# Kernel optimization log

Hardware: AMD Instinct MI355X
Metric: run time of the kernel (lower is better)

Reference implementation:

```python
import jax, jax.numpy as jnp
import numpy as np

NEG_SLOPE = 0.2


def gat_conv(h_in, src, dst, W, attn_l, attn_r, num_nodes):
    """DGL-style GATConv: fc -> per-head attention logits -> edge softmax over dst -> scatter-add."""
    H, D = attn_l.shape
    h = (h_in @ W).reshape(num_nodes, H, D)                      # [N,H,D]
    el = jnp.sum(h * attn_l, axis=-1)                            # [N,H]
    er = jnp.sum(h * attn_r, axis=-1)                            # [N,H]
    e = jax.nn.leaky_relu(el[src] + er[dst], NEG_SLOPE)          # [E,H]
    m = jax.ops.segment_max(e, dst, num_segments=num_nodes)      # [N,H]
    m = jnp.where(jnp.isfinite(m), m, 0.0)                       # guard empty segments
    ex = jnp.exp(e - m[dst])                                     # [E,H]
    denom = jax.ops.segment_sum(ex, dst, num_segments=num_nodes) # [N,H]
    a = ex / denom[dst]                                          # [E,H]
    msg = h[src] * a[:, :, None]                                 # [E,H,D]
    out = jax.ops.segment_sum(msg, dst, num_segments=num_nodes)  # [N,H,D]
    return out.reshape(num_nodes, H * D)                         # concat heads


def setup_inputs() -> dict:
    key = jax.random.key(0)
    ks = jax.random.split(key, 12)
    N, E, G = 65536, 1048576, 512
    F_in, H, D = 128, 8, 32
    F_mid = H * D  # 256, concat agg mode
    P = 512
    inp = {
        "node_feats": jax.random.normal(ks[0], (N, F_in), jnp.float32),
        "src": jax.random.randint(ks[1], (E,), 0, N, jnp.int32),
        "dst": jax.random.randint(ks[2], (E,), 0, N, jnp.int32),
        "graph_ids": jnp.sort(jax.random.randint(ks[3], (N,), 0, G, jnp.int32)),
        "num_graphs": G,
        "W0": jax.random.normal(ks[4], (F_in, H * D), jnp.float32) * (1.0 / np.sqrt(F_in)),
        "al0": jax.random.normal(ks[5], (H, D), jnp.float32) * 0.1,
        "ar0": jax.random.normal(ks[6], (H, D), jnp.float32) * 0.1,
        "W1": jax.random.normal(ks[7], (F_mid, H * D), jnp.float32) * (1.0 / np.sqrt(F_mid)),
        "al1": jax.random.normal(ks[8], (H, D), jnp.float32) * 0.1,
        "ar1": jax.random.normal(ks[9], (H, D), jnp.float32) * 0.1,
        "Wd1": jax.random.normal(ks[10], (F_mid, P), jnp.float32) * (1.0 / np.sqrt(F_mid)),
        "bd1": jnp.zeros((P,), jnp.float32),
        "Wd2": jax.random.normal(ks[11], (P, 1), jnp.float32) * (1.0 / np.sqrt(P)),
        "bd2": jnp.zeros((1,), jnp.float32),
    }
    return inp


def reference(node_feats, src, dst, graph_ids, num_graphs,
              W0, al0, ar0, W1, al1, ar1, Wd1, bd1, Wd2, bd2):
    N = node_feats.shape[0]
    # two GATConv message-passing steps with concat head aggregation
    h = gat_conv(node_feats, src, dst, W0, al0, ar0, N)   # [N, 256]
    h = gat_conv(h, src, dst, W1, al1, ar1, N)            # [N, 256]
    # mean readout per graph (AvgPooling)
    sums = jax.ops.segment_sum(h, graph_ids, num_segments=num_graphs)         # [G, 256]
    counts = jax.ops.segment_sum(jnp.ones((N,), h.dtype), graph_ids,
                                 num_segments=num_graphs)                     # [G]
    pooled = sums / jnp.maximum(counts, 1.0)[:, None]
    # predictor MLP: Dense(512, relu) -> Dense(1, linear)
    hidden = jax.nn.relu(pooled @ Wd1 + bd1)
    out = hidden @ Wd2 + bd2                               # [G, 1]
    return out
```

## Files before the change

kernel.cpp:

```cpp
#include <hip/hip_runtime.h>

#define LEAKY 0.2f

typedef unsigned short ushort_t;
typedef __attribute__((ext_vector_type(8))) short short8;
typedef __attribute__((ext_vector_type(4))) float f32x4;

__device__ __forceinline__ unsigned short f2bf(float f) {
  unsigned u = __float_as_uint(f);
  unsigned r = (u + 0x7fff + ((u >> 16) & 1)) >> 16;
  return (unsigned short)r;
}
__device__ __forceinline__ float bf2f(unsigned short u) {
  return __uint_as_float(((unsigned)u) << 16);
}

__global__ __launch_bounds__(256) void prep_k(int* __restrict__ cnt,
                                              const float* __restrict__ W0,
                                              const float* __restrict__ W1,
                                              ushort_t* __restrict__ W0h,
                                              ushort_t* __restrict__ W1h, int N) {
  int i = blockIdx.x * 256 + threadIdx.x;
  if (i < N) cnt[i] = 0;
  if (i < 256 * 128) {
    int k = i % 128, c = i / 128;
    W0h[i] = f2bf(W0[(long)k * 256 + c]);
  }
  if (i < 256 * 256) {
    int k = i % 256, c = i / 256;
    W1h[i] = f2bf(W1[(long)k * 256 + c]);
  }
}

__global__ void count_k(const int* __restrict__ dst, int* __restrict__ cnt,
                        int* __restrict__ slot, int E) {
  int base = (blockIdx.x * blockDim.x + threadIdx.x) * 4;
  if (base + 3 < E) {
    int4 d = *(const int4*)(dst + base);
    int4 s;
    s.x = atomicAdd(&cnt[d.x], 1);
    s.y = atomicAdd(&cnt[d.y], 1);
    s.z = atomicAdd(&cnt[d.z], 1);
    s.w = atomicAdd(&cnt[d.w], 1);
    *(int4*)(slot + base) = s;
  } else {
    for (int i = base; i < E; ++i) slot[i] = atomicAdd(&cnt[dst[i]], 1);
  }
}

__global__ __launch_bounds__(1024) void scan1_k(const int* __restrict__ cnt,
                                                int* __restrict__ ptr,
                                                int* __restrict__ bsum, int N) {
  int t = threadIdx.x;
  int i = blockIdx.x * 1024 + t;
  int v = (i < N) ? cnt[i] : 0;
  int lane = t & 63, w = t >> 6;
  int x = v;
  #pragma unroll
  for (int off = 1; off < 64; off <<= 1) {
    int y = __shfl_up(x, off, 64);
    if (lane >= off) x += y;
  }
  __shared__ int wsum[16];
  if (lane == 63) wsum[w] = x;
  __syncthreads();
  if (t < 16) {
    int s = wsum[t];
    #pragma unroll
    for (int off = 1; off < 16; off <<= 1) {
      int y = __shfl_up(s, off, 16);
      if (t >= off) s += y;
    }
    wsum[t] = s;
  }
  __syncthreads();
  int woff = (w > 0) ? wsum[w - 1] : 0;
  int incl = x + woff;
  if (i < N) ptr[i] = incl - v;
  if (t == 1023) bsum[blockIdx.x] = incl;
}

__global__ __launch_bounds__(1024) void scan23_k(int* __restrict__ ptr,
                                                 const int* __restrict__ bsum,
                                                 int nb, int N, int E) {
  __shared__ int sh[64];
  int t = threadIdx.x;
  if (t < 64) {
    int v = (t < nb) ? bsum[t] : 0;
    int x = v;
    #pragma unroll
    for (int off = 1; off < 64; off <<= 1) {
      int y = __shfl_up(x, off, 64);
      if (t >= off) x += y;
    }
    sh[t] = x - v;
  }
  __syncthreads();
  int i = blockIdx.x * 1024 + t;
  if (i < N) ptr[i] += sh[blockIdx.x];
  if (i == 0) ptr[N] = E;
}

__global__ void fill_k(const int* __restrict__ dst, const int* __restrict__ src,
                       const int* __restrict__ slot, const int* __restrict__ ptr,
                       int* __restrict__ adj, int E) {
  int base = (blockIdx.x * blockDim.x + threadIdx.x) * 4;
  if (base + 3 < E) {
    int4 d = *(const int4*)(dst + base);
    int4 s = *(const int4*)(src + base);
    int4 q = *(const int4*)(slot + base);
    adj[ptr[d.x] + q.x] = s.x;
    adj[ptr[d.y] + q.y] = s.y;
    adj[ptr[d.z] + q.z] = s.z;
    adj[ptr[d.w] + q.w] = s.w;
  } else {
    for (int i = base; i < E; ++i) adj[ptr[dst[i]] + slot[i]] = src[i];
  }
}

#define LDT 40
template <int AF32>
__global__ __launch_bounds__(256) void gemmT_k(const void* __restrict__ Ag_,
                                               const ushort_t* __restrict__ Bh,
                                               const float* __restrict__ alv,
                                               const float* __restrict__ arv,
                                               ushort_t* __restrict__ C,
                                               float* __restrict__ el,
                                               float* __restrict__ er,
                                               int N, int K) {
  __shared__ ushort_t smem[128 * LDT + 256 * LDT];
  ushort_t* As = smem;
  ushort_t* Bs = smem + 128 * LDT;
  int t = threadIdx.x;
  int w = t >> 6, l = t & 63;
  int wv_r = w >> 1, wv_c = w & 1;
  long row0 = (long)blockIdx.x * 128;
  int fr = l & 15;
  int ko = (l >> 4) * 8;
  int crow = (l >> 4) * 4;
  int ar = t >> 1;
  int ak = (t & 1) * 16;
  int bc = t;
  f32x4 acc[4][8] = {};

  for (int k0 = 0; k0 < K; k0 += 32) {
    ushort4 ha[4];
    uint4 a0, a1;
    if (AF32) {
      const float* ap = (const float*)Ag_ + (row0 + ar) * (long)K + k0 + ak;
      float4 v0 = *(const float4*)(ap + 0);
      float4 v1 = *(const float4*)(ap + 4);
      float4 v2 = *(const float4*)(ap + 8);
      float4 v3 = *(const float4*)(ap + 12);
      ha[0] = make_ushort4(f2bf(v0.x), f2bf(v0.y), f2bf(v0.z), f2bf(v0.w));
      ha[1] = make_ushort4(f2bf(v1.x), f2bf(v1.y), f2bf(v1.z), f2bf(v1.w));
      ha[2] = make_ushort4(f2bf(v2.x), f2bf(v2.y), f2bf(v2.z), f2bf(v2.w));
      ha[3] = make_ushort4(f2bf(v3.x), f2bf(v3.y), f2bf(v3.z), f2bf(v3.w));
    } else {
      const ushort_t* ap = (const ushort_t*)Ag_ + (row0 + ar) * (long)K + k0 + ak;
      a0 = *(const uint4*)ap;
      a1 = *(const uint4*)(ap + 8);
    }
    const ushort_t* bp = Bh + (long)bc * K + k0;
    uint4 b0 = *(const uint4*)bp;
    uint4 b1 = *(const uint4*)(bp + 8);
    uint4 b2 = *(const uint4*)(bp + 16);
    uint4 b3 = *(const uint4*)(bp + 24);
    __syncthreads();
    if (AF32) {
      *(ushort4*)&As[ar * LDT + ak + 0] = ha[0];
      *(ushort4*)&As[ar * LDT + ak + 4] = ha[1];
      *(ushort4*)&As[ar * LDT + ak + 8] = ha[2];
      *(ushort4*)&As[ar * LDT + ak + 12] = ha[3];
    } else {
      *(uint4*)&As[ar * LDT + ak] = a0;
      *(uint4*)&As[ar * LDT + ak + 8] = a1;
    }
    *(uint4*)&Bs[bc * LDT + 0] = b0;
    *(uint4*)&Bs[bc * LDT + 8] = b1;
    *(uint4*)&Bs[bc * LDT + 16] = b2;
    *(uint4*)&Bs[bc * LDT + 24] = b3;
    __syncthreads();
    short8 fah[4];
    #pragma unroll
    for (int m = 0; m < 4; ++m)
      fah[m] = *(const short8*)&As[(wv_r * 64 + m * 16 + fr) * LDT + ko];
    #pragma unroll
    for (int n = 0; n < 8; ++n) {
      short8 fb = *(const short8*)&Bs[(wv_c * 128 + n * 16 + fr) * LDT + ko];
      #pragma unroll
      for (int m = 0; m < 4; ++m)
        acc[m][n] = __builtin_amdgcn_mfma_f32_16x16x32_bf16(fah[m], fb, acc[m][n], 0, 0, 0);
    }
  }
  float ala[4], alb[4], ara[4], arb[4];
  #pragma unroll
  for (int hd = 0; hd < 4; ++hd) {
    int hbase = (wv_c * 4 + hd) * 32;
    ala[hd] = alv[hbase + fr];
    alb[hd] = alv[hbase + 16 + fr];
    ara[hd] = arv[hbase + fr];
    arb[hd] = arv[hbase + 16 + fr];
  }
  #pragma unroll
  for (int m = 0; m < 4; ++m) {
    #pragma unroll
    for (int r = 0; r < 4; ++r) {
      long row = row0 + wv_r * 64 + m * 16 + crow + r;
      #pragma unroll
      for (int n = 0; n < 8; ++n)
        C[row * 256 + wv_c * 128 + n * 16 + fr] = f2bf(acc[m][n][r]);
      #pragma unroll
      for (int hd = 0; hd < 4; ++hd) {
        float pel = acc[m][2 * hd][r] * ala[hd] + acc[m][2 * hd + 1][r] * alb[hd];
        float per = acc[m][2 * hd][r] * ara[hd] + acc[m][2 * hd + 1][r] * arb[hd];
        #pragma unroll
        for (int s = 1; s < 16; s <<= 1) {
          pel += __shfl_xor(pel, s);
          per += __shfl_xor(per, s);
        }
        if (fr == 0) {
          el[row * 8 + wv_c * 4 + hd] = pel;
          er[row * 8 + wv_c * 4 + hd] = per;
        }
      }
    }
  }
}

__global__ __launch_bounds__(256) void agg_k(const ushort_t* __restrict__ hb,
                                             const float* __restrict__ el,
                                             const float* __restrict__ er,
                                             const int* __restrict__ ptr,
                                             const int* __restrict__ adj,
                                             ushort_t* __restrict__ oh, int N) {
  __shared__ float2 att[4][64][8];
  int wid = threadIdx.x >> 6;
  int l = threadIdx.x & 63;
  int n = blockIdx.x * 4 + wid;
  if (n >= N) return;
  int beg = ptr[n];
  int deg = ptr[n + 1] - beg;
  long obase = (long)n * 256 + l * 4;
  float4 acc = make_float4(0.f, 0.f, 0.f, 0.f);
  if (deg > 0) {
    int hh = l & 7;
    int eo = l >> 3;
    int hg = l >> 3;
    float erv = er[(long)n * 8 + hh];
    if (deg <= 64) {
      int sid = (l < deg) ? adj[beg + l] : 0;
      int npass = (deg + 7) >> 3;
      float v[8];
      int sv[8];
      float m = -1e30f;
      #pragma unroll
      for (int p = 0; p < 8; ++p) {
        if (p < npass) {
          int e = p * 8 + eo;
          int s = __shfl(sid, e);
          sv[p] = s;
          float vv = -1e30f;
          if (e < deg) {
            vv = el[(long)s * 8 + hh] + erv;
            vv = fmaxf(vv, LEAKY * vv);
          }
          v[p] = vv;
          m = fmaxf(m, vv);
        }
      }
      m = fmaxf(m, __shfl_xor(m, 8));
      m = fmaxf(m, __shfl_xor(m, 16));
      m = fmaxf(m, __shfl_xor(m, 32));
      float ssum = 0.f;
      #pragma unroll
      for (int p = 0; p < 8; ++p) {
        if (p < npass) {
          float ex = (p * 8 + eo < deg) ? __expf(v[p] - m) : 0.f;
          v[p] = ex;
          ssum += ex;
        }
      }
      ssum += __shfl_xor(ssum, 8);
      ssum += __shfl_xor(ssum, 16);
      ssum += __shfl_xor(ssum, 32);
      float inv = 1.0f / ssum;
      #pragma unroll
      for (int p = 0; p < 8; ++p) {
        if (p < npass) {
          int e = p * 8 + eo;
          if (e < deg)
            att[wid][e][hh] = make_float2(v[p] * inv, __int_as_float(sv[p]));
        }
      }
      for (int p = 0; p < npass; ++p) {
        #pragma unroll
        for (int e2 = 0; e2 < 8; ++e2) {
          int e = p * 8 + e2;
          if (e < deg) {
            float2 as_ = att[wid][e][hg];
            float a = as_.x;
            int s = __float_as_int(as_.y);
            const ushort4 hv = *(const ushort4*)(hb + (long)s * 256 + l * 4);
            acc.x += a * bf2f(hv.x);
            acc.y += a * bf2f(hv.y);
            acc.z += a * bf2f(hv.z);
            acc.w += a * bf2f(hv.w);
          }
        }
      }
    } else {
      float m = -1e30f;
      for (int base = 0; base < deg; base += 8) {
        int e = base + eo;
        float vv = -1e30f;
        if (e < deg) {
          int s = adj[beg + e];
          vv = el[(long)s * 8 + hh] + erv;
          vv = fmaxf(vv, LEAKY * vv);
        }
        m = fmaxf(m, vv);
      }
      m = fmaxf(m, __shfl_xor(m, 8));
      m = fmaxf(m, __shfl_xor(m, 16));
      m = fmaxf(m, __shfl_xor(m, 32));
      float ssum = 0.f;
      for (int base = 0; base < deg; base += 8) {
        int e = base + eo;
        if (e < deg) {
          int s = adj[beg + e];
          float vv = el[(long)s * 8 + hh] + erv;
          vv = fmaxf(vv, LEAKY * vv);
          ssum += __expf(vv - m);
        }
      }
      ssum += __shfl_xor(ssum, 8);
      ssum += __shfl_xor(ssum, 16);
      ssum += __shfl_xor(ssum, 32);
      float inv = 1.0f / ssum;
      for (int base = 0; base < deg; base += 8) {
        int e = base + eo;
        float a_me = 0.f;
        int s_me = 0;
        if (e < deg) {
          s_me = adj[beg + e];
          float vv = el[(long)s_me * 8 + hh] + erv;
          vv = fmaxf(vv, LEAKY * vv);
          a_me = __expf(vv - m) * inv;
        }
        #pragma unroll
        for (int e2 = 0; e2 < 8; ++e2) {
          int e3 = base + e2;
          if (e3 < deg) {
            int srcl = (e2 << 3) | hg;
            float a = __shfl(a_me, srcl);
            int s = __shfl(s_me, srcl);
            const ushort4 hv = *(const ushort4*)(hb + (long)s * 256 + l * 4);
            acc.x += a * bf2f(hv.x);
            acc.y += a * bf2f(hv.y);
            acc.z += a * bf2f(hv.z);
            acc.w += a * bf2f(hv.w);
          }
        }
      }
    }
  }
  *(ushort4*)(oh + obase) =
      make_ushort4(f2bf(acc.x), f2bf(acc.y), f2bf(acc.z), f2bf(acc.w));
}

__device__ __forceinline__ int lower_bound_i(const int* a, int n, int key) {
  int lo = 0, hi = n;
  while (lo < hi) {
    int mid = (lo + hi) >> 1;
    if (a[mid] < key) lo = mid + 1; else hi = mid;
  }
  return lo;
}

__global__ __launch_bounds__(256) void poolmlp_k(const ushort_t* __restrict__ h,
                                                 const int* __restrict__ gid,
                                                 const float* __restrict__ Wd1,
                                                 const float* __restrict__ bd1,
                                                 const float* __restrict__ Wd2,
                                                 const float* __restrict__ bd2,
                                                 float* __restrict__ outv, int N, int G) {
  int g = blockIdx.x;
  int t = threadIdx.x;
  __shared__ int s_lo, s_hi;
  if (t == 0) {
    s_lo = lower_bound_i(gid, N, g);
    s_hi = lower_bound_i(gid, N, g + 1);
  }
  __syncthreads();
  int lo = s_lo, hi = s_hi;
  float acc = 0.f;
  for (int n = lo; n < hi; ++n) acc += bf2f(h[(long)n * 256 + t]);
  float c = (float)(hi - lo);
  __shared__ float p_s[256];
  __shared__ float red[256];
  p_s[t] = acc / fmaxf(c, 1.f);
  __syncthreads();
  float acc0 = bd1[t], acc1 = bd1[t + 256];
  for (int k = 0; k < 256; ++k) {
    float pv = p_s[k];
    acc0 += pv * Wd1[k * 512 + t];
    acc1 += pv * Wd1[k * 512 + t + 256];
  }
  acc0 = fmaxf(acc0, 0.f);
  acc1 = fmaxf(acc1, 0.f);
  red[t] = acc0 * Wd2[t] + acc1 * Wd2[t + 256];
  __syncthreads();
  for (int off = 128; off > 0; off >>= 1) {
    if (t < off) red[t] += red[t + off];
    __syncthreads();
  }
  if (t == 0) outv[g] = red[0] + bd2[0];
}

extern "C" void kernel_launch(void* const* d_in, const int* in_sizes, int n_in,
                              void* d_out, int out_size, void* d_ws, size_t ws_size,
                              hipStream_t stream) {
  const float* X   = (const float*)d_in[0];
  const int*   src = (const int*)d_in[1];
  const int*   dst = (const int*)d_in[2];
  const int*   gid = (const int*)d_in[3];
  const float* W0  = (const float*)d_in[5];
  const float* al0 = (const float*)d_in[6];
  const float* ar0 = (const float*)d_in[7];
  const float* W1  = (const float*)d_in[8];
  const float* al1 = (const float*)d_in[9];
  const float* ar1 = (const float*)d_in[10];
  const float* Wd1 = (const float*)d_in[11];
  const float* bd1 = (const float*)d_in[12];
  const float* Wd2 = (const float*)d_in[13];
  const float* bd2 = (const float*)d_in[14];

  int E = in_sizes[1];
  int N = in_sizes[3];
  int G = out_size;

  char* p = (char*)d_ws;
  ushort_t* hb   = (ushort_t*)p; p += (size_t)N * 256 * 2;
  ushort_t* hagg = (ushort_t*)p; p += (size_t)N * 256 * 2;
  float*    el   = (float*)p;    p += (size_t)N * 8 * 4;
  float*    er   = (float*)p;    p += (size_t)N * 8 * 4;
  ushort_t* W0h  = (ushort_t*)p; p += (size_t)256 * 128 * 2;
  ushort_t* W1h  = (ushort_t*)p; p += (size_t)256 * 256 * 2;
  int*      ptr  = (int*)p;      p += (size_t)(N + 1) * 4;
  int*      cnt  = (int*)p;      p += (size_t)N * 4;
  int*      adj  = (int*)p;      p += (size_t)E * 4;
  int*      slot = (int*)p;      p += (size_t)E * 4;
  int*      bsum = (int*)p;

  int nb = (N + 1023) / 1024;

  prep_k<<<(N + 255) / 256, 256, 0, stream>>>(cnt, W0, W1, W0h, W1h, N);
  count_k<<<(E / 4 + 255) / 256, 256, 0, stream>>>(dst, cnt, slot, E);
  scan1_k<<<nb, 1024, 0, stream>>>(cnt, ptr, bsum, N);
  scan23_k<<<nb, 1024, 0, stream>>>(ptr, bsum, nb, N, E);
  fill_k<<<(E / 4 + 255) / 256, 256, 0, stream>>>(dst, src, slot, ptr, adj, E);

  gemmT_k<1><<<N / 128, 256, 0, stream>>>((const void*)X, W0h, al0, ar0, hb, el, er, N, 128);
  agg_k<<<(N + 3) / 4, 256, 0, stream>>>(hb, el, er, ptr, adj, hagg, N);
  gemmT_k<0><<<N / 128, 256, 0, stream>>>((const void*)hagg, W1h, al1, ar1, hb, el, er, N, 256);
  agg_k<<<(N + 3) / 4, 256, 0, stream>>>(hb, el, er, ptr, adj, hagg, N);
  poolmlp_k<<<G, 256, 0, stream>>>(hagg, gid, Wd1, bd1, Wd2, bd2, (float*)d_out, N, G);
}
```

Before: 415.5 us.

## Merge adjacency fill into first GEMM launch and use shuffles in aggregation

The CSR fill kernel becomes extra blocks inside the first GEMM launch, which removes one launch and lets the fill overlap with the GEMM. In the aggregation kernel, the low-degree path now broadcasts attention weights and source ids through wave shuffles instead of staging them in LDS, which frees shared memory and drops a store/load round trip. The pooling loop is unrolled by four with independent accumulators to expose more memory-level parallelism. The leaky ReLU is rewritten as a select. Fill blocks still reserve the GEMM's shared-memory allocation, which may limit how many can be resident at once.

```diff
diff --git a/kernel.cpp b/kernel.cpp
--- a/kernel.cpp
+++ b/kernel.cpp
@@ -101,25 +101,8 @@
   if (i == 0) ptr[N] = E;
 }
 
-__global__ void fill_k(const int* __restrict__ dst, const int* __restrict__ src,
-                       const int* __restrict__ slot, const int* __restrict__ ptr,
-                       int* __restrict__ adj, int E) {
-  int base = (blockIdx.x * blockDim.x + threadIdx.x) * 4;
-  if (base + 3 < E) {
-    int4 d = *(const int4*)(dst + base);
-    int4 s = *(const int4*)(src + base);
-    int4 q = *(const int4*)(slot + base);
-    adj[ptr[d.x] + q.x] = s.x;
-    adj[ptr[d.y] + q.y] = s.y;
-    adj[ptr[d.z] + q.z] = s.z;
-    adj[ptr[d.w] + q.w] = s.w;
-  } else {
-    for (int i = base; i < E; ++i) adj[ptr[dst[i]] + slot[i]] = src[i];
-  }
-}
-
 #define LDT 40
-template <int AF32>
+template <int AF32, int FILL>
 __global__ __launch_bounds__(256) void gemmT_k(const void* __restrict__ Ag_,
                                                const ushort_t* __restrict__ Bh,
                                                const float* __restrict__ alv,
@@ -127,8 +110,28 @@
                                                ushort_t* __restrict__ C,
                                                float* __restrict__ el,
                                                float* __restrict__ er,
-                                               int N, int K) {
+                                               int N, int K, int gemmBlocks,
+                                               const int* __restrict__ dstv,
+                                               const int* __restrict__ srcv,
+                                               const int* __restrict__ slot,
+                                               const int* __restrict__ ptrc,
+                                               int* __restrict__ adj, int E) {
   __shared__ ushort_t smem[128 * LDT + 256 * LDT];
+  if (FILL && blockIdx.x >= gemmBlocks) {
+    int base = ((blockIdx.x - gemmBlocks) * 256 + threadIdx.x) * 4;
+    if (base + 3 < E) {
+      int4 d = *(const int4*)(dstv + base);
+      int4 s = *(const int4*)(srcv + base);
+      int4 q = *(const int4*)(slot + base);
+      adj[ptrc[d.x] + q.x] = s.x;
+      adj[ptrc[d.y] + q.y] = s.y;
+      adj[ptrc[d.z] + q.z] = s.z;
+      adj[ptrc[d.w] + q.w] = s.w;
+    } else {
+      for (int i = base; i < E; ++i) adj[ptrc[dstv[i]] + slot[i]] = srcv[i];
+    }
+    return;
+  }
   ushort_t* As = smem;
   ushort_t* Bs = smem + 128 * LDT;
   int t = threadIdx.x;
@@ -234,7 +237,6 @@
                                              const int* __restrict__ ptr,
                                              const int* __restrict__ adj,
                                              ushort_t* __restrict__ oh, int N) {
-  __shared__ float2 att[4][64][8];
   int wid = threadIdx.x >> 6;
   int l = threadIdx.x & 63;
   int n = blockIdx.x * 4 + wid;
@@ -252,18 +254,16 @@
       int sid = (l < deg) ? adj[beg + l] : 0;
       int npass = (deg + 7) >> 3;
       float v[8];
-      int sv[8];
       float m = -1e30f;
       #pragma unroll
       for (int p = 0; p < 8; ++p) {
         if (p < npass) {
           int e = p * 8 + eo;
           int s = __shfl(sid, e);
-          sv[p] = s;
           float vv = -1e30f;
           if (e < deg) {
             vv = el[(long)s * 8 + hh] + erv;
-            vv = fmaxf(vv, LEAKY * vv);
+            vv = vv > 0.f ? vv : LEAKY * vv;
           }
           v[p] = vv;
           m = fmaxf(m, vv);
@@ -288,24 +288,19 @@
       #pragma unroll
       for (int p = 0; p < 8; ++p) {
         if (p < npass) {
-          int e = p * 8 + eo;
-          if (e < deg)
-            att[wid][e][hh] = make_float2(v[p] * inv, __int_as_float(sv[p]));
-        }
-      }
-      for (int p = 0; p < npass; ++p) {
-        #pragma unroll
-        for (int e2 = 0; e2 < 8; ++e2) {
-          int e = p * 8 + e2;
-          if (e < deg) {
-            float2 as_ = att[wid][e][hg];
-            float a = as_.x;
-            int s = __float_as_int(as_.y);
-            const ushort4 hv = *(const ushort4*)(hb + (long)s * 256 + l * 4);
-            acc.x += a * bf2f(hv.x);
-            acc.y += a * bf2f(hv.y);
-            acc.z += a * bf2f(hv.z);
-            acc.w += a * bf2f(hv.w);
+          v[p] *= inv;
+          #pragma unroll
+          for (int e2 = 0; e2 < 8; ++e2) {
+            int e = p * 8 + e2;
+            if (e < deg) {
+              float a = __shfl(v[p], (e2 << 3) | hg);
+              int s = __shfl(sid, e);
+              const ushort4 hv = *(const ushort4*)(hb + (long)s * 256 + l * 4);
+              acc.x += a * bf2f(hv.x);
+              acc.y += a * bf2f(hv.y);
+              acc.z += a * bf2f(hv.z);
+              acc.w += a * bf2f(hv.w);
+            }
           }
         }
       }
@@ -317,7 +312,7 @@
         if (e < deg) {
           int s = adj[beg + e];
           vv = el[(long)s * 8 + hh] + erv;
-          vv = fmaxf(vv, LEAKY * vv);
+          vv = vv > 0.f ? vv : LEAKY * vv;
         }
         m = fmaxf(m, vv);
       }
@@ -330,7 +325,7 @@
         if (e < deg) {
           int s = adj[beg + e];
           float vv = el[(long)s * 8 + hh] + erv;
-          vv = fmaxf(vv, LEAKY * vv);
+          vv = vv > 0.f ? vv : LEAKY * vv;
           ssum += __expf(vv - m);
         }
       }
@@ -345,7 +340,7 @@
         if (e < deg) {
           s_me = adj[beg + e];
           float vv = el[(long)s_me * 8 + hh] + erv;
-          vv = fmaxf(vv, LEAKY * vv);
+          vv = vv > 0.f ? vv : LEAKY * vv;
           a_me = __expf(vv - m) * inv;
         }
         #pragma unroll
@@ -394,8 +389,16 @@
   }
   __syncthreads();
   int lo = s_lo, hi = s_hi;
-  float acc = 0.f;
-  for (int n = lo; n < hi; ++n) acc += bf2f(h[(long)n * 256 + t]);
+  float a0 = 0.f, a1 = 0.f, a2 = 0.f, a3 = 0.f;
+  int n = lo;
+  for (; n + 3 < hi; n += 4) {
+    a0 += bf2f(h[(long)(n + 0) * 256 + t]);
+    a1 += bf2f(h[(long)(n + 1) * 256 + t]);
+    a2 += bf2f(h[(long)(n + 2) * 256 + t]);
+    a3 += bf2f(h[(long)(n + 3) * 256 + t]);
+  }
+  for (; n < hi; ++n) a0 += bf2f(h[(long)n * 256 + t]);
+  float acc = (a0 + a1) + (a2 + a3);
   float c = (float)(hi - lo);
   __shared__ float p_s[256];
   __shared__ float red[256];
@@ -454,16 +457,21 @@
   int*      bsum = (int*)p;
 
   int nb = (N + 1023) / 1024;
+  int gemmBlocks = N / 128;
+  int fillBlocks = (E / 4 + 255) / 256;
 
   prep_k<<<(N + 255) / 256, 256, 0, stream>>>(cnt, W0, W1, W0h, W1h, N);
   count_k<<<(E / 4 + 255) / 256, 256, 0, stream>>>(dst, cnt, slot, E);
   scan1_k<<<nb, 1024, 0, stream>>>(cnt, ptr, bsum, N);
   scan23_k<<<nb, 1024, 0, stream>>>(ptr, bsum, nb, N, E);
-  fill_k<<<(E / 4 + 255) / 256, 256, 0, stream>>>(dst, src, slot, ptr, adj, E);
-
-  gemmT_k<1><<<N / 128, 256, 0, stream>>>((const void*)X, W0h, al0, ar0, hb, el, er, N, 128);
+
+  gemmT_k<1, 1><<<gemmBlocks + fillBlocks, 256, 0, stream>>>(
+      (const void*)X, W0h, al0, ar0, hb, el, er, N, 128, gemmBlocks,
+      dst, src, slot, ptr, adj, E);
   agg_k<<<(N + 3) / 4, 256, 0, stream>>>(hb, el, er, ptr, adj, hagg, N);
-  gemmT_k<0><<<N / 128, 256, 0, stream>>>((const void*)hagg, W1h, al1, ar1, hb, el, er, N, 256);
+  gemmT_k<0, 0><<<gemmBlocks, 256, 0, stream>>>(
+      (const void*)hagg, W1h, al1, ar1, hb, el, er, N, 256, gemmBlocks,
+      nullptr, nullptr, nullptr, nullptr, nullptr, 0);
   agg_k<<<(N + 3) / 4, 256, 0, stream>>>(hb, el, er, ptr, adj, hagg, N);
   poolmlp_k<<<G, 256, 0, stream>>>(hagg, gid, Wd1, bd1, Wd2, bd2, (float*)d_out, N, G);
 }
```

New measurement: 383.3 us. 7.7% less time.
